# Performance work log

Measured on AMD Instinct MI355X. Metric: run time of the kernel, lower is better.

## Reference

```python
import jax, jax.numpy as jnp
import numpy as np

N_NODES, N_EDGES, D = 20000, 320000, 256

def mish(x):
    return x * jnp.tanh(jax.nn.softplus(x))

def setup_inputs() -> dict:
    key = jax.random.key(0)
    ks = jax.random.split(key, 12)
    s = 1.0 / np.sqrt(D)
    return {
        "node_features": jax.random.normal(ks[0], (N_NODES, D), jnp.float32),
        "edge_features": jax.random.normal(ks[1], (N_EDGES, D), jnp.float32),
        "targets": jax.random.normal(ks[2], (N_NODES, 1), jnp.float32),
        "src": jax.random.randint(ks[3], (N_EDGES,), 0, N_NODES),
        "dst": jax.random.randint(ks[4], (N_EDGES,), 0, N_NODES),
        "W_dense": jax.random.uniform(ks[5], (D, D), jnp.float32, -s, s),
        "b_dense": jax.random.uniform(ks[6], (D,), jnp.float32, -s, s),
        "W_edge": jax.random.uniform(ks[7], (D, D), jnp.float32, -s, s),
        "b_edge": jax.random.uniform(ks[8], (D,), jnp.float32, -s, s),
        "W_out": jax.random.uniform(ks[9], (D, D), jnp.float32, -s, s),
        "b_out": jax.random.uniform(ks[10], (D,), jnp.float32, -s, s),
    }

def reference(node_features, edge_features, targets, src, dst,
              W_dense, b_dense, W_edge, b_edge, W_out, b_out):
    # node / edge MLP projections with Mish
    x = mish(node_features @ W_dense.T + b_dense)          # [N, D]
    y = mish(edge_features @ W_edge.T + b_edge)            # [E, D]
    # GINEConv (apply_func=None, eps=0): (1+eps)*x + sum_{(u->v)} relu(x_u + e_uv)
    msg = jax.nn.relu(x[src] + y)                          # [E, D] gather + combine
    agg = jax.ops.segment_sum(msg, dst, num_segments=node_features.shape[0])
    rst = x + agg                                          # eps = 0
    return mish(rst @ W_out.T + b_out)
```

## Files before the change

### kernel.cpp

```cpp
#include <hip/hip_runtime.h>
#include <hip/hip_bf16.h>

#define DD 256
#define TROWS 16
#define BSTRIDE 264

typedef __attribute__((ext_vector_type(8))) short bf16x8;
typedef __attribute__((ext_vector_type(4))) float f32x4;

__device__ __forceinline__ unsigned cvt_pk_bf16(float lo, float hi) {
    unsigned r;
    asm("v_cvt_pk_bf16_f32 %0, %1, %2" : "=v"(r) : "v"(lo), "v"(hi));
    return r;
}

__device__ __forceinline__ ushort f2bf(float f) {
    unsigned u = __float_as_uint(f);
    u += 0x7fffu + ((u >> 16) & 1u);
    return (ushort)(u >> 16);
}
__device__ __forceinline__ float bf2f(ushort h) {
    return __uint_as_float(((unsigned)h) << 16);
}

__device__ __forceinline__ float mish_f(float t) {
    float u = __expf(t);
    float w = u * (u + 2.0f);
    float r = t * w * __builtin_amdgcn_rcpf(w + 2.0f);
    return (t > 15.0f) ? t : r;
}

__device__ __forceinline__ void stage16(const float* __restrict__ src, size_t rowStride,
                                        int rowsValid, char* lds) {
    const int t = threadIdx.x;
#pragma unroll
    for (int i = 0; i < 2; ++i) {
        int c = i * 256 + t;
        int row = c >> 5;
        int col8 = (c & 31) << 3;
        float4 va = make_float4(0.f, 0.f, 0.f, 0.f);
        float4 vb = va;
        if (row < rowsValid) {
            const float* p = src + (size_t)row * rowStride + col8;
            va = *(const float4*)p;
            vb = *(const float4*)(p + 4);
        }
        uint4 h;
        h.x = cvt_pk_bf16(va.x, va.y);
        h.y = cvt_pk_bf16(va.z, va.w);
        h.z = cvt_pk_bf16(vb.x, vb.y);
        h.w = cvt_pk_bf16(vb.z, vb.w);
        int off = row * 512 + ((((c & 31) << 4)) ^ ((row & 7) << 4));
        *(uint4*)(lds + off) = h;
    }
}

__device__ __forceinline__ void gemm16(const char* lds, const ushort* __restrict__ Wf,
                                       f32x4 acc[4]) {
    const int lane = threadIdx.x & 63;
    const int wave = threadIdx.x >> 6;
    const int arow = lane & 15;
    const int halfk = lane >> 4;
    const int ctg0 = wave * 4;
    const bf16x8* Wfrag = (const bf16x8*)Wf;
#pragma unroll
    for (int ks = 0; ks < 8; ++ks) {
        int kbyte = ks * 64 + halfk * 16;
        bf16x8 a = *(const bf16x8*)(lds + arow * 512 + (kbyte ^ ((arow & 7) << 4)));
#pragma unroll
        for (int ct = 0; ct < 4; ++ct) {
            bf16x8 b = Wfrag[((ctg0 + ct) * 8 + ks) * 64 + lane];
            acc[ct] = __builtin_amdgcn_mfma_f32_16x16x32_bf16(a, b, acc[ct], 0, 0, 0);
        }
    }
}

__global__ void __launch_bounds__(256) convert_w_kernel(const float* __restrict__ in,
                                                        ushort* __restrict__ out, int nfrag) {
    int f = blockIdx.x * blockDim.x + threadIdx.x;
    if (f >= nfrag) return;
    int lane = f & 63;
    int ks = (f >> 6) & 7;
    int ct = f >> 9;
    int row = ct * 16 + (lane & 15);
    int kbase = ks * 32 + (lane >> 4) * 8;
    const float* p = in + (size_t)row * DD + kbase;
    float4 a = *(const float4*)p;
    float4 b = *(const float4*)(p + 4);
    ushort4 h0, h1;
    h0.x = f2bf(a.x); h0.y = f2bf(a.y); h0.z = f2bf(a.z); h0.w = f2bf(a.w);
    h1.x = f2bf(b.x); h1.y = f2bf(b.y); h1.z = f2bf(b.z); h1.w = f2bf(b.w);
    ushort4* o = (ushort4*)(out + (size_t)f * 8);
    o[0] = h0; o[1] = h1;
}

__global__ void __launch_bounds__(256) zero_kernel(int* __restrict__ p, int n) {
    int i = blockIdx.x * blockDim.x + threadIdx.x;
    if (i < n) p[i] = 0;
}

__global__ void __launch_bounds__(256) hist_kernel(const int* __restrict__ dst,
                                                   int* __restrict__ h, int E) {
    int e = blockIdx.x * blockDim.x + threadIdx.x;
    if (e < E) atomicAdd(&h[dst[e]], 1);
}

__global__ void __launch_bounds__(256) scan1_kernel(const int* __restrict__ h,
                                                    int* __restrict__ excl,
                                                    int* __restrict__ bsum, int n) {
    __shared__ int wsum[4];
    const int lane = threadIdx.x & 63;
    const int wave = threadIdx.x >> 6;
    int i = blockIdx.x * 256 + threadIdx.x;
    int v = (i < n) ? h[i] : 0;
    int s = v;
#pragma unroll
    for (int off = 1; off < 64; off <<= 1) {
        int u = __shfl_up(s, off, 64);
        if (lane >= off) s += u;
    }
    if (lane == 63) wsum[wave] = s;
    __syncthreads();
    int prefix = 0;
    for (int wv = 0; wv < wave; ++wv) prefix += wsum[wv];
    if (i < n) excl[i] = prefix + s - v;
    if (threadIdx.x == 255) bsum[blockIdx.x] = prefix + s;
}

__global__ void __launch_bounds__(256) scan2_kernel(int* __restrict__ bsum, int nb) {
    __shared__ int wsum[4];
    const int lane = threadIdx.x & 63;
    const int wave = threadIdx.x >> 6;
    int i = threadIdx.x;
    int v = (i < nb) ? bsum[i] : 0;
    int s = v;
#pragma unroll
    for (int off = 1; off < 64; off <<= 1) {
        int u = __shfl_up(s, off, 64);
        if (lane >= off) s += u;
    }
    if (lane == 63) wsum[wave] = s;
    __syncthreads();
    int prefix = 0;
    for (int wv = 0; wv < wave; ++wv) prefix += wsum[wv];
    if (i < nb) bsum[i] = prefix + s - v;
}

__global__ void __launch_bounds__(256) scan3_kernel(int* __restrict__ excl,
                                                    const int* __restrict__ bsum, int n) {
    int i = blockIdx.x * 256 + threadIdx.x;
    if (i < n) excl[i] += bsum[blockIdx.x];
}

__global__ void __launch_bounds__(256) scatter_kernel(const int* __restrict__ src,
                                                      const int* __restrict__ dst,
                                                      int* __restrict__ h2,
                                                      int* __restrict__ permS,
                                                      int* __restrict__ srcS,
                                                      int* __restrict__ dstS, int E) {
    int e = blockIdx.x * blockDim.x + threadIdx.x;
    if (e < E) {
        int d = dst[e];
        int pos = atomicAdd(&h2[d], 1);
        permS[pos] = e;
        srcS[pos] = src[e];
        dstS[pos] = d;
    }
}

__global__ void __launch_bounds__(256, 8) node_kernel(const float* __restrict__ nf,
                                                      const ushort* __restrict__ Wd,
                                                      const float* __restrict__ bd,
                                                      ushort* __restrict__ xbf,
                                                      float* __restrict__ agg, int M) {
    __shared__ char lds[TROWS * 512];
    const int base = blockIdx.x * TROWS;
    const int rowsValid = min(TROWS, M - base);
    stage16(nf + (size_t)base * DD, DD, rowsValid, lds);
    __syncthreads();
    f32x4 acc[4];
#pragma unroll
    for (int i = 0; i < 4; ++i) acc[i] = (f32x4){0.f, 0.f, 0.f, 0.f};
    gemm16(lds, Wd, acc);
    const int lane = threadIdx.x & 63;
    const int wave = threadIdx.x >> 6;
    const int colBase = wave * 64;
    const int r = lane & 15, q = lane >> 4;
#pragma unroll
    for (int ct = 0; ct < 4; ++ct) {
        int col = colBase + ct * 16 + r;
        float bb = bd[col];
#pragma unroll
        for (int j = 0; j < 4; ++j) {
            int lrow = q * 4 + j;
            if (lrow < rowsValid) {
                size_t idx = (size_t)(base + lrow) * DD + col;
                float m = mish_f(acc[ct][j] + bb);
                xbf[idx] = (ushort)cvt_pk_bf16(m, m);
                agg[idx] = m;
            }
        }
    }
}

__global__ void __launch_bounds__(256, 8) edge_kernel(const float* __restrict__ ef,
                                                      const ushort* __restrict__ We,
                                                      const float* __restrict__ be,
                                                      const ushort* __restrict__ xbf,
                                                      const int* __restrict__ permS,
                                                      const int* __restrict__ srcS,
                                                      const int* __restrict__ dstS,
                                                      float* __restrict__ agg, int E) {
    __shared__ char smem[TROWS * BSTRIDE * 2];
    __shared__ int permRow[TROWS];
    __shared__ int srcRow[TROWS];
    __shared__ int dstRow[TROWS];

    const int t = threadIdx.x;
    const int base = blockIdx.x * TROWS;
    const int rowsValid = min(TROWS, E - base);

    if (t < TROWS) {
        int gi = base + t;
        int gic = (gi < E) ? gi : (E - 1);
        permRow[t] = permS[gic];
        srcRow[t] = srcS[gic];
        dstRow[t] = (gi < E) ? dstS[gic] : -1;
    }
    __syncthreads();

#pragma unroll
    for (int i = 0; i < 2; ++i) {
        int c = i * 256 + t;
        int row = c >> 5;
        int col8 = (c & 31) << 3;
        float4 va = make_float4(0.f, 0.f, 0.f, 0.f);
        float4 vb = va;
        if (row < rowsValid) {
            const float* p = ef + (size_t)permRow[row] * DD + col8;
            va = *(const float4*)p;
            vb = *(const float4*)(p + 4);
        }
        uint4 h;
        h.x = cvt_pk_bf16(va.x, va.y);
        h.y = cvt_pk_bf16(va.z, va.w);
        h.z = cvt_pk_bf16(vb.x, vb.y);
        h.w = cvt_pk_bf16(vb.z, vb.w);
        int off = row * 512 + ((((c & 31) << 4)) ^ ((row & 7) << 4));
        *(uint4*)(smem + off) = h;
    }
    __syncthreads();

    f32x4 acc[4];
#pragma unroll
    for (int i = 0; i < 4; ++i) acc[i] = (f32x4){0.f, 0.f, 0.f, 0.f};
    gemm16(smem, We, acc);
    __syncthreads();

    ushort* xt = (ushort*)smem;
#pragma unroll
    for (int i = 0; i < 2; ++i) {
        int c = i * 256 + t;
        int row = c >> 5;
        int col8 = (c & 31) << 3;
        int4 v = make_int4(0, 0, 0, 0);
        if (row < rowsValid)
            v = *(const int4*)(xbf + (size_t)srcRow[row] * DD + col8);
        *(int4*)(xt + row * BSTRIDE + col8) = v;
    }
    __syncthreads();

    const int lane = t & 63;
    const int wave = t >> 6;
    const int colBase = wave * 64;
    const int r = lane & 15, q = lane >> 4;
#pragma unroll
    for (int ct = 0; ct < 4; ++ct) {
        int col = colBase + ct * 16 + r;
        float bb = be[col];
#pragma unroll
        for (int j = 0; j < 4; ++j) {
            int lrow = q * 4 + j;
            float y = mish_f(acc[ct][j] + bb);
            float xval = bf2f(xt[lrow * BSTRIDE + col]);
            float msg = (lrow < rowsValid) ? fmaxf(xval + y, 0.f) : 0.f;
            xt[lrow * BSTRIDE + col] = (ushort)cvt_pk_bf16(msg, msg);
        }
    }
    __syncthreads();

    {
        int col = t;
        float run = 0.f;
        int dprev = dstRow[0];
#pragma unroll
        for (int r2 = 0; r2 < TROWS; ++r2) {
            int d = dstRow[r2];
            if (d != dprev) {
                if (dprev >= 0) atomicAdd(agg + (size_t)dprev * DD + col, run);
                run = 0.f;
                dprev = d;
            }
            run += bf2f(xt[r2 * BSTRIDE + col]);
        }
        if (dprev >= 0) atomicAdd(agg + (size_t)dprev * DD + col, run);
    }
}

__global__ void __launch_bounds__(256, 8) out_kernel(const ushort* __restrict__ Wo,
                                                     const float* __restrict__ bo,
                                                     float* __restrict__ agg_out, int M) {
    __shared__ char lds[TROWS * 512];
    const int base = blockIdx.x * TROWS;
    const int rowsValid = min(TROWS, M - base);
    stage16(agg_out + (size_t)base * DD, DD, rowsValid, lds);
    __syncthreads();
    f32x4 acc[4];
#pragma unroll
    for (int i = 0; i < 4; ++i) acc[i] = (f32x4){0.f, 0.f, 0.f, 0.f};
    gemm16(lds, Wo, acc);
    const int lane = threadIdx.x & 63;
    const int wave = threadIdx.x >> 6;
    const int colBase = wave * 64;
    const int r = lane & 15, q = lane >> 4;
#pragma unroll
    for (int ct = 0; ct < 4; ++ct) {
        int col = colBase + ct * 16 + r;
        float bb = bo[col];
#pragma unroll
        for (int j = 0; j < 4; ++j) {
            int lrow = q * 4 + j;
            if (lrow < rowsValid) {
                size_t idx = (size_t)(base + lrow) * DD + col;
                agg_out[idx] = mish_f(acc[ct][j] + bb);
            }
        }
    }
}

extern "C" void kernel_launch(void* const* d_in, const int* in_sizes, int n_in,
                              void* d_out, int out_size, void* d_ws, size_t ws_size,
                              hipStream_t stream) {
    const float* nf = (const float*)d_in[0];
    const float* ef = (const float*)d_in[1];
    const int* src = (const int*)d_in[3];
    const int* dst = (const int*)d_in[4];
    const float* Wd = (const float*)d_in[5];
    const float* bd = (const float*)d_in[6];
    const float* We = (const float*)d_in[7];
    const float* be = (const float*)d_in[8];
    const float* Wo = (const float*)d_in[9];
    const float* bo = (const float*)d_in[10];

    const int M = in_sizes[0] / DD;
    const int E = in_sizes[1] / DD;
    float* out = (float*)d_out;

    auto align = [](size_t v) { return (v + 255) & ~(size_t)255; };
    char* ws = (char*)d_ws;
    size_t off = 0;
    ushort* xbf = (ushort*)(ws + off); off += align((size_t)M * DD * 2);
    ushort* Wdb = (ushort*)(ws + off); off += align((size_t)DD * DD * 2);
    ushort* Web = (ushort*)(ws + off); off += align((size_t)DD * DD * 2);
    ushort* Wob = (ushort*)(ws + off); off += align((size_t)DD * DD * 2);
    int* h     = (int*)(ws + off); off += align((size_t)M * 4);
    int* h2    = (int*)(ws + off); off += align((size_t)M * 4);
    int* bsum  = (int*)(ws + off); off += align(256 * 4);
    int* permS = (int*)(ws + off); off += align((size_t)E * 4);
    int* srcS  = (int*)(ws + off); off += align((size_t)E * 4);
    int* dstS  = (int*)(ws + off); off += align((size_t)E * 4);

    const int nfrag = (DD / 16) * (DD / 32) * 64;
    convert_w_kernel<<<(nfrag + 255) / 256, 256, 0, stream>>>(Wd, Wdb, nfrag);
    convert_w_kernel<<<(nfrag + 255) / 256, 256, 0, stream>>>(We, Web, nfrag);
    convert_w_kernel<<<(nfrag + 255) / 256, 256, 0, stream>>>(Wo, Wob, nfrag);

    const int nbScan = (M + 255) / 256;
    zero_kernel<<<(M + 255) / 256, 256, 0, stream>>>(h, M);
    hist_kernel<<<(E + 255) / 256, 256, 0, stream>>>(dst, h, E);
    scan1_kernel<<<nbScan, 256, 0, stream>>>(h, h2, bsum, M);
    scan2_kernel<<<1, 256, 0, stream>>>(bsum, nbScan);
    scan3_kernel<<<nbScan, 256, 0, stream>>>(h2, bsum, M);
    scatter_kernel<<<(E + 255) / 256, 256, 0, stream>>>(src, dst, h2, permS, srcS, dstS, E);

    const int nwgN = (M + TROWS - 1) / TROWS;
    node_kernel<<<nwgN, 256, 0, stream>>>(nf, Wdb, bd, xbf, out, M);
    const int nwgE = (E + TROWS - 1) / TROWS;
    edge_kernel<<<nwgE, 256, 0, stream>>>(ef, Web, be, xbf, permS, srcS, dstS, out, E);
    out_kernel<<<nwgN, 256, 0, stream>>>(Wob, bo, out, M);
}
```

Baseline: 278.0 us.

## Make edge kernel persistent with double-buffered prefetch of edge tiles

The edge kernel becomes a persistent grid-stride loop over 16-row edge tiles, launched with 2048 blocks. While the current tile's GEMM runs, each block prefetches the next tile's edge-feature rows into registers, gathers the source-node rows, and loads the indices two tiles ahead, using rotating LDS buffers. The goal is to hide global-load latency behind the MFMA work and cut block launch overhead. In exchange it uses more registers and LDS per block and adds synchronization, which may lower occupancy.

```diff
diff --git a/kernel.cpp b/kernel.cpp
--- a/kernel.cpp
+++ b/kernel.cpp
@@ -4,6 +4,7 @@
 #define DD 256
 #define TROWS 16
 #define BSTRIDE 264
+#define SBYTES (TROWS * 528)
 
 typedef __attribute__((ext_vector_type(8))) short bf16x8;
 typedef __attribute__((ext_vector_type(4))) float f32x4;
@@ -210,100 +211,168 @@
                                                       const int* __restrict__ permS,
                                                       const int* __restrict__ srcS,
                                                       const int* __restrict__ dstS,
-                                                      float* __restrict__ agg, int E) {
-    __shared__ char smem[TROWS * BSTRIDE * 2];
-    __shared__ int permRow[TROWS];
-    __shared__ int srcRow[TROWS];
-    __shared__ int dstRow[TROWS];
+                                                      float* __restrict__ agg,
+                                                      int E, int nTiles) {
+    __shared__ char stage[2][SBYTES];
+    __shared__ int idxP[3][TROWS], idxS[3][TROWS], idxD[3][TROWS];
 
     const int t = threadIdx.x;
-    const int base = blockIdx.x * TROWS;
-    const int rowsValid = min(TROWS, E - base);
-
-    if (t < TROWS) {
-        int gi = base + t;
-        int gic = (gi < E) ? gi : (E - 1);
-        permRow[t] = permS[gic];
-        srcRow[t] = srcS[gic];
-        dstRow[t] = (gi < E) ? dstS[gic] : -1;
-    }
-    __syncthreads();
-
-#pragma unroll
-    for (int i = 0; i < 2; ++i) {
-        int c = i * 256 + t;
-        int row = c >> 5;
-        int col8 = (c & 31) << 3;
-        float4 va = make_float4(0.f, 0.f, 0.f, 0.f);
-        float4 vb = va;
-        if (row < rowsValid) {
-            const float* p = ef + (size_t)permRow[row] * DD + col8;
-            va = *(const float4*)p;
-            vb = *(const float4*)(p + 4);
-        }
-        uint4 h;
-        h.x = cvt_pk_bf16(va.x, va.y);
-        h.y = cvt_pk_bf16(va.z, va.w);
-        h.z = cvt_pk_bf16(vb.x, vb.y);
-        h.w = cvt_pk_bf16(vb.z, vb.w);
-        int off = row * 512 + ((((c & 31) << 4)) ^ ((row & 7) << 4));
-        *(uint4*)(smem + off) = h;
-    }
-    __syncthreads();
-
-    f32x4 acc[4];
-#pragma unroll
-    for (int i = 0; i < 4; ++i) acc[i] = (f32x4){0.f, 0.f, 0.f, 0.f};
-    gemm16(smem, We, acc);
-    __syncthreads();
-
-    ushort* xt = (ushort*)smem;
-#pragma unroll
-    for (int i = 0; i < 2; ++i) {
-        int c = i * 256 + t;
-        int row = c >> 5;
-        int col8 = (c & 31) << 3;
-        int4 v = make_int4(0, 0, 0, 0);
-        if (row < rowsValid)
-            v = *(const int4*)(xbf + (size_t)srcRow[row] * DD + col8);
-        *(int4*)(xt + row * BSTRIDE + col8) = v;
-    }
-    __syncthreads();
-
+    const int G = gridDim.x;
     const int lane = t & 63;
     const int wave = t >> 6;
     const int colBase = wave * 64;
     const int r = lane & 15, q = lane >> 4;
-#pragma unroll
-    for (int ct = 0; ct < 4; ++ct) {
-        int col = colBase + ct * 16 + r;
-        float bb = be[col];
-#pragma unroll
-        for (int j = 0; j < 4; ++j) {
-            int lrow = q * 4 + j;
-            float y = mish_f(acc[ct][j] + bb);
-            float xval = bf2f(xt[lrow * BSTRIDE + col]);
-            float msg = (lrow < rowsValid) ? fmaxf(xval + y, 0.f) : 0.f;
-            xt[lrow * BSTRIDE + col] = (ushort)cvt_pk_bf16(msg, msg);
-        }
+
+    int tile = blockIdx.x;
+    if (tile >= nTiles) return;
+
+    if (t < TROWS) {
+        int gi = tile * TROWS + t;
+        int gic = min(gi, E - 1);
+        idxP[0][t] = permS[gic];
+        idxS[0][t] = srcS[gic];
+        idxD[0][t] = (gi < E) ? dstS[gic] : -1;
     }
     __syncthreads();
 
+    float4 va[2], vb[2];
     {
-        int col = t;
-        float run = 0.f;
-        int dprev = dstRow[0];
-#pragma unroll
-        for (int r2 = 0; r2 < TROWS; ++r2) {
-            int d = dstRow[r2];
-            if (d != dprev) {
-                if (dprev >= 0) atomicAdd(agg + (size_t)dprev * DD + col, run);
-                run = 0.f;
-                dprev = d;
-            }
-            run += bf2f(xt[r2 * BSTRIDE + col]);
-        }
-        if (dprev >= 0) atomicAdd(agg + (size_t)dprev * DD + col, run);
+        int rv0 = min(TROWS, E - tile * TROWS);
+#pragma unroll
+        for (int i = 0; i < 2; ++i) {
+            int c = i * 256 + t;
+            int row = c >> 5;
+            int col8 = (c & 31) << 3;
+            va[i] = make_float4(0.f, 0.f, 0.f, 0.f);
+            vb[i] = va[i];
+            if (row < rv0) {
+                const float* p = ef + (size_t)idxP[0][row] * DD + col8;
+                va[i] = *(const float4*)p;
+                vb[i] = *(const float4*)(p + 4);
+            }
+        }
+    }
+    int pN = 0, sN = 0, dN = -1;
+    {
+        int nextTile = tile + G;
+        if (t < TROWS && nextTile < nTiles) {
+            int gi = nextTile * TROWS + t;
+            int gic = min(gi, E - 1);
+            pN = permS[gic];
+            sN = srcS[gic];
+            dN = (gi < E) ? dstS[gic] : -1;
+        }
+    }
+
+    int k = 0;
+    for (; tile < nTiles; tile += G, ++k) {
+        const int cur = k & 1;
+        const int ic = k % 3;
+        const int inx = (k + 1) % 3;
+        const int nextTile = tile + G;
+        const int rv = min(TROWS, E - tile * TROWS);
+        const int rvN = (nextTile < nTiles) ? min(TROWS, E - nextTile * TROWS) : 0;
+
+#pragma unroll
+        for (int i = 0; i < 2; ++i) {
+            int c = i * 256 + t;
+            int row = c >> 5;
+            uint4 h;
+            h.x = cvt_pk_bf16(va[i].x, va[i].y);
+            h.y = cvt_pk_bf16(va[i].z, va[i].w);
+            h.z = cvt_pk_bf16(vb[i].x, vb[i].y);
+            h.w = cvt_pk_bf16(vb[i].z, vb[i].w);
+            int off = row * 512 + ((((c & 31) << 4)) ^ ((row & 7) << 4));
+            *(uint4*)(stage[cur] + off) = h;
+        }
+        if (t < TROWS && nextTile < nTiles) {
+            idxP[inx][t] = pN;
+            idxS[inx][t] = sN;
+            idxD[inx][t] = dN;
+        }
+        __syncthreads();
+
+#pragma unroll
+        for (int i = 0; i < 2; ++i) {
+            int c = i * 256 + t;
+            int row = c >> 5;
+            int col8 = (c & 31) << 3;
+            va[i] = make_float4(0.f, 0.f, 0.f, 0.f);
+            vb[i] = va[i];
+            if (row < rvN) {
+                const float* p = ef + (size_t)idxP[inx][row] * DD + col8;
+                va[i] = *(const float4*)p;
+                vb[i] = *(const float4*)(p + 4);
+            }
+        }
+        int4 xv[2];
+#pragma unroll
+        for (int i = 0; i < 2; ++i) {
+            int c = i * 256 + t;
+            int row = c >> 5;
+            int col8 = (c & 31) << 3;
+            xv[i] = make_int4(0, 0, 0, 0);
+            if (row < rv)
+                xv[i] = *(const int4*)(xbf + (size_t)idxS[ic][row] * DD + col8);
+        }
+        {
+            int nnTile = tile + 2 * G;
+            pN = 0; sN = 0; dN = -1;
+            if (t < TROWS && nnTile < nTiles) {
+                int gi = nnTile * TROWS + t;
+                int gic = min(gi, E - 1);
+                pN = permS[gic];
+                sN = srcS[gic];
+                dN = (gi < E) ? dstS[gic] : -1;
+            }
+        }
+        f32x4 acc[4];
+#pragma unroll
+        for (int i = 0; i < 4; ++i) acc[i] = (f32x4){0.f, 0.f, 0.f, 0.f};
+        gemm16(stage[cur], We, acc);
+        __syncthreads();
+
+        ushort* xt = (ushort*)stage[cur];
+#pragma unroll
+        for (int i = 0; i < 2; ++i) {
+            int c = i * 256 + t;
+            int row = c >> 5;
+            int col8 = (c & 31) << 3;
+            *(int4*)(xt + row * BSTRIDE + col8) = xv[i];
+        }
+        __syncthreads();
+
+#pragma unroll
+        for (int ct = 0; ct < 4; ++ct) {
+            int col = colBase + ct * 16 + r;
+            float bb = be[col];
+#pragma unroll
+            for (int j = 0; j < 4; ++j) {
+                int lrow = q * 4 + j;
+                float y = mish_f(acc[ct][j] + bb);
+                float xval = bf2f(xt[lrow * BSTRIDE + col]);
+                float msg = (lrow < rv) ? fmaxf(xval + y, 0.f) : 0.f;
+                xt[lrow * BSTRIDE + col] = (ushort)cvt_pk_bf16(msg, msg);
+            }
+        }
+        __syncthreads();
+
+        {
+            int col = t;
+            float run = 0.f;
+            int dprev = idxD[ic][0];
+#pragma unroll
+            for (int r2 = 0; r2 < TROWS; ++r2) {
+                int d = idxD[ic][r2];
+                if (d != dprev) {
+                    if (dprev >= 0) atomicAdd(agg + (size_t)dprev * DD + col, run);
+                    run = 0.f;
+                    dprev = d;
+                }
+                run += bf2f(xt[r2 * BSTRIDE + col]);
+            }
+            if (dprev >= 0) atomicAdd(agg + (size_t)dprev * DD + col, run);
+        }
     }
 }
 
@@ -385,7 +454,11 @@
 
     const int nwgN = (M + TROWS - 1) / TROWS;
     node_kernel<<<nwgN, 256, 0, stream>>>(nf, Wdb, bd, xbf, out, M);
-    const int nwgE = (E + TROWS - 1) / TROWS;
-    edge_kernel<<<nwgE, 256, 0, stream>>>(ef, Web, be, xbf, permS, srcS, dstS, out, E);
+
+    const int nTiles = (E + TROWS - 1) / TROWS;
+    int gridE = 256 * 8;
+    if (gridE > nTiles) gridE = nTiles;
+    edge_kernel<<<gridE, 256, 0, stream>>>(ef, Web, be, xbf, permS, srcS, dstS, out, E, nTiles);
+
     out_kernel<<<nwgN, 256, 0, stream>>>(Wob, bo, out, M);
 }
```

New measurement: 499.1 us. +79.5%, slower.
